# Kernel optimization log

Hardware: AMD Instinct MI355X
Metric: run time of the kernel (lower is better)

## Reference

```python
import jax, jax.numpy as jnp
import numpy as np

ALL_PERMS = jnp.array([[0, 1, 2], [0, 2, 1], [1, 0, 2], [1, 2, 0], [2, 0, 1], [2, 1, 0]], dtype=jnp.int32)
ENRICH_CLIP = 100.0
B, D, H = 16384, 512, 512
P_IN = D + 6 + 3   # seq_embed + pres_state(6) + round_onehot(3)
F_IN = D + 12 + 3  # seq_embed + full_state(12) + round_onehot(3)


def _gelu(x):
    return jax.nn.gelu(x, approximate=False)  # keras 'gelu' is erf-based


def _mlp3(x, w1, b1, w2, b2, w3, b3):
    h = _gelu(x @ w1 + b1)
    h = _gelu(h @ w2 + b2)
    return h @ w3 + b3


def setup_inputs() -> dict:
    key = jax.random.key(0)
    ks = jax.random.split(key, 12)
    s = 0.02
    return {
        'seq_embed': jax.random.normal(ks[0], (B, D), jnp.float32),
        'freq': jax.random.normal(ks[1], (B, 3), jnp.float32),
        'pres': (jax.random.uniform(ks[2], (B, 3)) < 0.5).astype(jnp.float32),
        'enrich': jax.random.normal(ks[3], (B, 3), jnp.float32),
        'pw1': jax.random.normal(ks[4], (P_IN, H), jnp.float32) * s, 'pb1': jnp.zeros((H,), jnp.float32),
        'pw2': jax.random.normal(ks[5], (H, H // 2), jnp.float32) * s, 'pb2': jnp.zeros((H // 2,), jnp.float32),
        'pw3': jax.random.normal(ks[6], (H // 2, 1), jnp.float32) * s, 'pb3': jnp.zeros((1,), jnp.float32),
        'fw1': jax.random.normal(ks[7], (F_IN, H), jnp.float32) * s, 'fb1': jnp.zeros((H,), jnp.float32),
        'fw2': jax.random.normal(ks[8], (H, H), jnp.float32) * s, 'fb2': jnp.zeros((H,), jnp.float32),
        'fw3': jax.random.normal(ks[9], (H, 2), jnp.float32) * s, 'fb3': jnp.zeros((2,), jnp.float32),
        'perm_idx': jax.random.randint(ks[10], (B,), 0, 6, dtype=jnp.int32),
        'round_mask': jax.random.randint(ks[11], (B, 3), 0, 2, dtype=jnp.int32),
    }


def _decode(seq_embed, freq, pres, enrich, mask_f, perms,
            pw1, pb1, pw2, pb2, pw3, pb3, fw1, fb1, fw2, fb2, fw3, fb3):
    Bn = seq_embed.shape[0]
    dt = seq_embed.dtype
    ones = jnp.ones((Bn,), dt)
    pres_state = jnp.zeros((Bn, 3, 2), dt)  # [R, (pres, decoded_flag)]
    full_state = jnp.zeros((Bn, 3, 4), dt)  # [R, (freq, pres, enrich, decoded_flag)]
    d_f = jnp.zeros((Bn, 3), dt)
    d_p = jnp.zeros((Bn, 3), dt)
    d_e = jnp.zeros((Bn, 3), dt)
    lf = lp = le = nm = jnp.float32(0.0)
    for step in range(3):
        ridx = perms[:, step]                               # [B]
        r_oh = jax.nn.one_hot(ridx, 3, dtype=dt)            # [B,3]
        take = lambda a: jnp.take_along_axis(a, ridx[:, None], axis=1)[:, 0]
        gt_f, gt_p, gt_e, m = take(freq), take(pres), take(enrich), take(mask_f)
        pres_inp = jnp.concatenate([seq_embed, pres_state.reshape(Bn, 6), r_oh], axis=1)
        pp_logit = _mlp3(pres_inp, pw1, pb1, pw2, pb2, pw3, pb3)[:, 0]
        fe_inp = jnp.concatenate([seq_embed, full_state.reshape(Bn, 12), r_oh], axis=1)
        fe_pred = _mlp3(fe_inp, fw1, fb1, fw2, fb2, fw3, fb3)
        pf, pe = fe_pred[:, 0], fe_pred[:, 1]
        lf = lf + jnp.sum(jnp.square(pf - gt_f) * m)
        bce = jnp.maximum(pp_logit, 0.0) - pp_logit * gt_p + jnp.log1p(jnp.exp(-jnp.abs(pp_logit)))
        lp = lp + jnp.sum(bce * m)
        le = le + jnp.sum(jnp.square(pe - gt_e) * m)
        nm = nm + jnp.sum(m)
        msk = m > 0.5
        act_f = jnp.where(msk, jnp.clip(pf, -10.0, 10.0), gt_f)
        act_p = jnp.where(msk, jax.nn.sigmoid(pp_logit), gt_p)
        act_e = jnp.where(msk, jnp.clip(pe, -ENRICH_CLIP, ENRICH_CLIP), gt_e)
        sel = r_oh[:, :, None]  # equal-mask scatter into the ridx-th slot
        pres_state = pres_state * (1.0 - sel) + jnp.stack([act_p, ones], axis=1)[:, None, :] * sel
        full_state = full_state * (1.0 - sel) + jnp.stack([act_f, act_p, act_e, ones], axis=1)[:, None, :] * sel
        d_f = d_f * (1.0 - r_oh) + act_f[:, None] * r_oh
        d_p = d_p * (1.0 - r_oh) + act_p[:, None] * r_oh
        d_e = d_e * (1.0 - r_oh) + act_e[:, None] * r_oh
    nm = nm + 1e-08
    return lf / nm, lp / nm, le / nm, d_f, d_p, d_e


def reference(seq_embed, freq, pres, enrich,
              pw1, pb1, pw2, pb2, pw3, pb3,
              fw1, fb1, fw2, fb2, fw3, fb3,
              perm_idx, round_mask):
    perms = ALL_PERMS[perm_idx]                      # [B,3] random round orders
    mask_f = round_mask.astype(seq_embed.dtype)      # [B,3] 0/1 mask
    lf, lp, le, d_f, d_p, d_e = _decode(seq_embed, freq, pres, enrich, mask_f, perms,
                                        pw1, pb1, pw2, pb2, pw3, pb3,
                                        fw1, fb1, fw2, fb2, fw3, fb3)
    # flat layout: [loss_freq, loss_pres, loss_enrich, dec_freq(B*3), dec_pres(B*3), dec_enrich(B*3)]
    return jnp.concatenate([jnp.stack([lf, lp, le]), d_f.ravel(), d_p.ravel(), d_e.ravel()])
```

## Files before the change

kernel.cpp:

```cpp
#include <hip/hip_runtime.h>
#include <hip/hip_bf16.h>
#include <math.h>

#define BATCH 16384

typedef unsigned short u16;
typedef short bf16x8 __attribute__((ext_vector_type(8)));
typedef float f32x4 __attribute__((ext_vector_type(4)));
typedef u16 u16x8 __attribute__((ext_vector_type(8)));
typedef u16 u16x4 __attribute__((ext_vector_type(4)));

__constant__ int PERMS_C[6][3] = {{0,1,2},{0,2,1},{1,0,2},{1,2,0},{2,0,1},{2,1,0}};

__device__ inline float bf2f(u16 u) {
    unsigned int x = ((unsigned int)u) << 16;
    float f; __builtin_memcpy(&f, &x, 4); return f;
}
__device__ inline u16 f2bf(float f) {
    __hip_bfloat16 h = __float2bfloat16(f);
    u16 u; __builtin_memcpy(&u, &h, 2); return u;
}
__device__ inline float gelu_exact(float x) {
    return 0.5f * x * (1.0f + erff(x * 0.70710678118654752f));
}

__device__ inline void gload_lds16(const u16* g, u16* l) {
    __builtin_amdgcn_global_load_lds(
        (const __attribute__((address_space(1))) unsigned int*)g,
        (__attribute__((address_space(3))) unsigned int*)l,
        16, 0, 0);
}

__global__ __launch_bounds__(256) void prep_kernel(
    const float* __restrict__ seq,
    const float* __restrict__ pw1, const float* __restrict__ pw2,
    const float* __restrict__ fw1, const float* __restrict__ fw2,
    const float* __restrict__ pb1, const float* __restrict__ pb2,
    const float* __restrict__ fb1, const float* __restrict__ fb2,
    u16* __restrict__ sb, u16* __restrict__ W1T, u16* __restrict__ W2T,
    float* __restrict__ bias1, float* __restrict__ bias2,
    float* __restrict__ states)
{
    const int N0 = BATCH * 512;
    const int N1 = 1024 * 512;
    const int N2 = 768 * 512;
    const int N3 = 1024;
    const int N4 = 768;
    const int N5 = BATCH * 18;
    int i = blockIdx.x * 256 + threadIdx.x;
    if (i < N0) { sb[i] = f2bf(seq[i]); return; }
    i -= N0;
    if (i < N1) {
        int n = i >> 9, k = i & 511;
        float v = (n < 512) ? pw1[(size_t)k * 512 + n] : fw1[(size_t)k * 512 + (n - 512)];
        W1T[i] = f2bf(v); return;
    }
    i -= N1;
    if (i < N2) {
        int n = i >> 9, k = i & 511;
        float v = (n < 256) ? pw2[(size_t)k * 256 + n] : fw2[(size_t)k * 512 + (n - 256)];
        W2T[i] = f2bf(v); return;
    }
    i -= N2;
    if (i < N3) { bias1[i] = (i < 512) ? pb1[i] : fb1[i - 512]; return; }
    i -= N3;
    if (i < N4) { bias2[i] = (i < 256) ? pb2[i] : fb2[i - 256]; return; }
    i -= N4;
    if (i < N5) { states[i] = 0.0f; return; }
}

__global__ __launch_bounds__(256) void gemm_bf16(
    const u16* __restrict__ A0, const u16* __restrict__ A1, int lda,
    const u16* __restrict__ Bt, const float* __restrict__ bias,
    u16* __restrict__ C, int M, int N, int K, int n_split, int apply_gelu)
{
    __shared__ __align__(16) u16 As[128 * 64];
    __shared__ __align__(16) u16 Bs[128 * 64];

    const int bm = blockIdx.x * 128;
    const int bn = blockIdx.y * 128;
    const u16* __restrict__ A = (bn < n_split) ? A0 : A1;

    const int tid = threadIdx.x;
    const int wv = tid >> 6;
    const int lane = tid & 63;
    const int wr = wv >> 1;
    const int wc = wv & 1;

    const int lrow = lane >> 3;
    const int lcol = (lane & 7) << 3;

    f32x4 acc[4][4];
#pragma unroll
    for (int i = 0; i < 4; ++i)
#pragma unroll
        for (int j = 0; j < 4; ++j) acc[i][j] = (f32x4){0.f, 0.f, 0.f, 0.f};

    for (int k0 = 0; k0 < K; k0 += 64) {
#pragma unroll
        for (int q = 0; q < 4; ++q) {
            const int c = wv * 4 + q;
            const int row = c * 8 + lrow;
            gload_lds16(&A[(size_t)(bm + row) * lda + k0 + lcol], &As[c * 512]);
            gload_lds16(&Bt[(size_t)(bn + row) * K + k0 + lcol], &Bs[c * 512]);
        }
        __syncthreads();

#pragma unroll
        for (int ks = 0; ks < 64; ks += 32) {
            int kk = ks + (lane >> 4) * 8;
            bf16x8 af[4], bfr[4];
#pragma unroll
            for (int i = 0; i < 4; ++i)
                af[i] = *reinterpret_cast<const bf16x8*>(&As[(wr * 64 + i * 16 + (lane & 15)) * 64 + kk]);
#pragma unroll
            for (int j = 0; j < 4; ++j)
                bfr[j] = *reinterpret_cast<const bf16x8*>(&Bs[(wc * 64 + j * 16 + (lane & 15)) * 64 + kk]);
#pragma unroll
            for (int i = 0; i < 4; ++i)
#pragma unroll
                for (int j = 0; j < 4; ++j)
                    acc[i][j] = __builtin_amdgcn_mfma_f32_16x16x32_bf16(af[i], bfr[j], acc[i][j], 0, 0, 0);
        }
        __syncthreads();
    }

    const int r4 = (lane >> 4) * 4;
    const int cn = lane & 15;
#pragma unroll
    for (int i = 0; i < 4; ++i) {
#pragma unroll
        for (int j = 0; j < 4; ++j) {
            int gcol = bn + wc * 64 + j * 16 + cn;
            float bsv = bias[gcol];
#pragma unroll
            for (int r = 0; r < 4; ++r) {
                int grow = bm + wr * 64 + i * 16 + r4 + r;
                float v = acc[i][j][r] + bsv;
                if (apply_gelu) v = gelu_exact(v);
                C[(size_t)grow * N + gcol] = f2bf(v);
            }
        }
    }
}

template<int NSTATE>
__device__ inline void step_h1_body(
    const u16* __restrict__ Z, const float* __restrict__ wsrc,
    const float* __restrict__ state, const int* __restrict__ perm_idx, int step,
    u16* __restrict__ H1, int colBase)
{
    constexpr int NR = NSTATE + 3;
    const int tid = threadIdx.x;
    const int c64 = tid & 63;
    const int ws = tid >> 6;
    const int col0 = c64 * 8;

    float w[NR][8];
#pragma unroll
    for (int t = 0; t < NR; ++t) {
        float4 a = *reinterpret_cast<const float4*>(&wsrc[(size_t)t * 512 + col0]);
        float4 b = *reinterpret_cast<const float4*>(&wsrc[(size_t)t * 512 + col0 + 4]);
        w[t][0] = a.x; w[t][1] = a.y; w[t][2] = a.z; w[t][3] = a.w;
        w[t][4] = b.x; w[t][5] = b.y; w[t][6] = b.z; w[t][7] = b.w;
    }

    int row = blockIdx.x * 16 + ws;
#pragma unroll 2
    for (int i = 0; i < 4; ++i, row += 4) {
        const int ridx = PERMS_C[perm_idx[row]][step];
        float s0[NSTATE];
        if constexpr (NSTATE == 6) {
            float2 a = *reinterpret_cast<const float2*>(&state[row * 6]);
            float2 b = *reinterpret_cast<const float2*>(&state[row * 6 + 2]);
            float2 c = *reinterpret_cast<const float2*>(&state[row * 6 + 4]);
            s0[0] = a.x; s0[1] = a.y; s0[2] = b.x; s0[3] = b.y; s0[4] = c.x; s0[5] = c.y;
        } else {
            float4 a = *reinterpret_cast<const float4*>(&state[row * 12]);
            float4 b = *reinterpret_cast<const float4*>(&state[row * 12 + 4]);
            float4 c = *reinterpret_cast<const float4*>(&state[row * 12 + 8]);
            s0[0] = a.x; s0[1] = a.y; s0[2]  = a.z; s0[3]  = a.w;
            s0[4] = b.x; s0[5] = b.y; s0[6]  = b.z; s0[7]  = b.w;
            s0[8] = c.x; s0[9] = c.y; s0[10] = c.z; s0[11] = c.w;
        }
        u16x8 z = *reinterpret_cast<const u16x8*>(&Z[(size_t)row * 1024 + colBase + col0]);
        u16x8 o;
#pragma unroll
        for (int e = 0; e < 8; ++e) {
            float d = (ridx == 0) ? w[NSTATE][e]
                    : ((ridx == 1) ? w[NSTATE + 1][e] : w[NSTATE + 2][e]);
#pragma unroll
            for (int t = 0; t < NSTATE; ++t) d += s0[t] * w[t][e];
            o[e] = f2bf(gelu_exact(bf2f(z[e]) + d));
        }
        *reinterpret_cast<u16x8*>(&H1[(size_t)row * 1024 + colBase + col0]) = o;
    }
}

__global__ __launch_bounds__(256) void step_h1_both(
    const u16* __restrict__ Z,
    const float* __restrict__ pw1s, const float* __restrict__ fw1s,
    const float* __restrict__ pres_state, const float* __restrict__ full_state,
    const int* __restrict__ perm_idx, int step, u16* __restrict__ H1)
{
    if (blockIdx.y == 0)
        step_h1_body<6>(Z, pw1s, pres_state, perm_idx, step, H1, 0);
    else
        step_h1_body<12>(Z, fw1s, full_state, perm_idx, step, H1, 512);
}

__global__ __launch_bounds__(256) void step_head(
    const u16* __restrict__ H2,
    const float* __restrict__ pw3, const float* __restrict__ pb3,
    const float* __restrict__ fw3, const float* __restrict__ fb3,
    const float* __restrict__ freq, const float* __restrict__ presv,
    const float* __restrict__ enrich,
    const int* __restrict__ round_mask, const int* __restrict__ perm_idx, int step,
    float* __restrict__ pres_state, float* __restrict__ full_state,
    float* __restrict__ part, float* __restrict__ out)
{
    const int wid = threadIdx.x >> 6;
    const int lane = threadIdx.x & 63;
    const int row0 = blockIdx.x * 16;

    __shared__ float lg[16][4];

    float4 wp = *reinterpret_cast<const float4*>(&pw3[lane * 4]);
    float4 wa = *reinterpret_cast<const float4*>(&fw3[lane * 16]);
    float4 wb = *reinterpret_cast<const float4*>(&fw3[lane * 16 + 4]);
    float4 wc = *reinterpret_cast<const float4*>(&fw3[lane * 16 + 8]);
    float4 wd = *reinterpret_cast<const float4*>(&fw3[lane * 16 + 12]);

#pragma unroll
    for (int i = 0; i < 4; ++i) {
        const int r = wid * 4 + i;
        const int b = row0 + r;
        const u16* h2 = &H2[(size_t)b * 768];

        u16x4 hp = *reinterpret_cast<const u16x4*>(&h2[lane * 4]);
        float sp = bf2f(hp[0]) * wp.x + bf2f(hp[1]) * wp.y
                 + bf2f(hp[2]) * wp.z + bf2f(hp[3]) * wp.w;

        u16x8 hf = *reinterpret_cast<const u16x8*>(&h2[256 + lane * 8]);
        float h0 = bf2f(hf[0]), h1 = bf2f(hf[1]), h2v = bf2f(hf[2]), h3 = bf2f(hf[3]);
        float h4 = bf2f(hf[4]), h5 = bf2f(hf[5]), h6v = bf2f(hf[6]), h7 = bf2f(hf[7]);
        float sf = h0 * wa.x + h1 * wa.z + h2v * wb.x + h3 * wb.z
                 + h4 * wc.x + h5 * wc.z + h6v * wd.x + h7 * wd.z;
        float se = h0 * wa.y + h1 * wa.w + h2v * wb.y + h3 * wb.w
                 + h4 * wc.y + h5 * wc.w + h6v * wd.y + h7 * wd.w;

        for (int off = 32; off > 0; off >>= 1) {
            sp += __shfl_down(sp, off);
            sf += __shfl_down(sf, off);
            se += __shfl_down(se, off);
        }
        if (lane == 0) { lg[r][0] = sp; lg[r][1] = sf; lg[r][2] = se; }
    }
    __syncthreads();

    float lf = 0.f, bce = 0.f, le = 0.f, mm = 0.f;
    if (wid == 0) {
        if (lane < 16) {
            const int b = row0 + lane;
            float logit = lg[lane][0] + pb3[0];
            float pf    = lg[lane][1] + fb3[0];
            float pe    = lg[lane][2] + fb3[1];
            int ridx = PERMS_C[perm_idx[b]][step];
            float gt_f = freq[b * 3 + ridx];
            float gt_p = presv[b * 3 + ridx];
            float gt_e = enrich[b * 3 + ridx];
            float m = (float)round_mask[b * 3 + ridx];
            lf  = (pf - gt_f) * (pf - gt_f) * m;
            bce = (fmaxf(logit, 0.f) - logit * gt_p + log1pf(expf(-fabsf(logit)))) * m;
            le  = (pe - gt_e) * (pe - gt_e) * m;
            mm  = m;
            bool msk = m > 0.5f;
            float act_f = msk ? fminf(fmaxf(pf, -10.f), 10.f) : gt_f;
            float act_p = msk ? 1.f / (1.f + expf(-logit)) : gt_p;
            float act_e = msk ? fminf(fmaxf(pe, -100.f), 100.f) : gt_e;
            pres_state[b * 6 + ridx * 2 + 0] = act_p;
            pres_state[b * 6 + ridx * 2 + 1] = 1.f;
            full_state[b * 12 + ridx * 4 + 0] = act_f;
            full_state[b * 12 + ridx * 4 + 1] = act_p;
            full_state[b * 12 + ridx * 4 + 2] = act_e;
            full_state[b * 12 + ridx * 4 + 3] = 1.f;
            out[3 + b * 3 + ridx] = act_f;
            out[3 + 3 * BATCH + b * 3 + ridx] = act_p;
            out[3 + 6 * BATCH + b * 3 + ridx] = act_e;
        }
        for (int off = 8; off > 0; off >>= 1) {
            lf  += __shfl_down(lf, off);
            bce += __shfl_down(bce, off);
            le  += __shfl_down(le, off);
            mm  += __shfl_down(mm, off);
        }
        if (lane == 0) {
            float4 v; v.x = lf; v.y = bce; v.z = le; v.w = mm;
            *reinterpret_cast<float4*>(&part[blockIdx.x * 4]) = v;
        }
    }
}

#define HEAD_BLOCKS (BATCH / 16)

__global__ __launch_bounds__(256) void finalize_kernel(
    const float* __restrict__ part, float* __restrict__ out)
{
    __shared__ float red[4][4];
    const int nslots = 3 * HEAD_BLOCKS;
    float a0 = 0.f, a1 = 0.f, a2 = 0.f, a3 = 0.f;
    for (int j = threadIdx.x; j < nslots; j += 256) {
        float4 v = *reinterpret_cast<const float4*>(&part[j * 4]);
        a0 += v.x; a1 += v.y; a2 += v.z; a3 += v.w;
    }
    for (int off = 32; off > 0; off >>= 1) {
        a0 += __shfl_down(a0, off);
        a1 += __shfl_down(a1, off);
        a2 += __shfl_down(a2, off);
        a3 += __shfl_down(a3, off);
    }
    const int wid = threadIdx.x >> 6, lane = threadIdx.x & 63;
    if (lane == 0) { red[wid][0] = a0; red[wid][1] = a1; red[wid][2] = a2; red[wid][3] = a3; }
    __syncthreads();
    if (threadIdx.x == 0) {
        float s0 = 0.f, s1 = 0.f, s2 = 0.f, s3 = 0.f;
#pragma unroll
        for (int w2 = 0; w2 < 4; ++w2) {
            s0 += red[w2][0]; s1 += red[w2][1]; s2 += red[w2][2]; s3 += red[w2][3];
        }
        float nm = s3 + 1e-8f;
        out[0] = s0 / nm;
        out[1] = s1 / nm;
        out[2] = s2 / nm;
    }
}

extern "C" void kernel_launch(void* const* d_in, const int* in_sizes, int n_in,
                              void* d_out, int out_size, void* d_ws, size_t ws_size,
                              hipStream_t stream)
{
    const float* seq       = (const float*)d_in[0];
    const float* freq      = (const float*)d_in[1];
    const float* presv     = (const float*)d_in[2];
    const float* enrich    = (const float*)d_in[3];
    const float* pw1       = (const float*)d_in[4];
    const float* pb1       = (const float*)d_in[5];
    const float* pw2       = (const float*)d_in[6];
    const float* pb2       = (const float*)d_in[7];
    const float* pw3       = (const float*)d_in[8];
    const float* pb3       = (const float*)d_in[9];
    const float* fw1       = (const float*)d_in[10];
    const float* fb1       = (const float*)d_in[11];
    const float* fw2       = (const float*)d_in[12];
    const float* fb2       = (const float*)d_in[13];
    const float* fw3       = (const float*)d_in[14];
    const float* fb3       = (const float*)d_in[15];
    const int*   perm_idx  = (const int*)d_in[16];
    const int*   round_mask= (const int*)d_in[17];
    float* out = (float*)d_out;

    char* w = (char*)d_ws;
    u16* sb  = (u16*)w;  w += (size_t)BATCH * 512 * 2;
    u16* Z   = (u16*)w;  w += (size_t)BATCH * 1024 * 2;
    u16* H1  = (u16*)w;  w += (size_t)BATCH * 1024 * 2;
    u16* H2  = (u16*)w;  w += (size_t)BATCH * 768 * 2;
    u16* W1T = (u16*)w;  w += (size_t)1024 * 512 * 2;
    u16* W2T = (u16*)w;  w += (size_t)768 * 512 * 2;
    float* bias1 = (float*)w; w += 1024 * 4;
    float* bias2 = (float*)w; w += 768 * 4;
    float* states = (float*)w; w += (size_t)BATCH * 18 * 4;
    float* part   = (float*)w;
    float* pres_state = states;
    float* full_state = states + (size_t)BATCH * 6;

    {
        const int total = BATCH * 512 + 1024 * 512 + 768 * 512 + 1024 + 768 + BATCH * 18;
        int grid = (total + 255) / 256;
        prep_kernel<<<grid, 256, 0, stream>>>(seq, pw1, pw2, fw1, fw2, pb1, pb2, fb1, fb2,
                                              sb, W1T, W2T, bias1, bias2, states);
    }

    gemm_bf16<<<dim3(BATCH / 128, 1024 / 128), 256, 0, stream>>>(
        sb, sb, 512, W1T, bias1, Z, BATCH, 1024, 512, 1 << 30, 0);

    for (int s = 0; s < 3; ++s) {
        step_h1_both<<<dim3(BATCH / 16, 2), 256, 0, stream>>>(
            Z, pw1 + (size_t)512 * 512, fw1 + (size_t)512 * 512,
            pres_state, full_state, perm_idx, s, H1);

        gemm_bf16<<<dim3(BATCH / 128, 768 / 128), 256, 0, stream>>>(
            H1, H1 + 512, 1024, W2T, bias2, H2, BATCH, 768, 512, 256, 1);

        step_head<<<HEAD_BLOCKS, 256, 0, stream>>>(
            H2, pw3, pb3, fw3, fb3, freq, presv, enrich,
            round_mask, perm_idx, s, pres_state, full_state,
            part + (size_t)s * HEAD_BLOCKS * 4, out);
    }

    finalize_kernel<<<1, 256, 0, stream>>>(part, out);
}
```

Before: 392.6 us.

## Double-buffer GEMM LDS tiles with swizzle and fuse step-0 H1 into first GEMM

The bf16 GEMM now uses two 32-wide K buffers in LDS. The next tile's global-to-LDS load is issued before the MFMA work on the current tile, with a manual vmcnt wait, and an XOR swizzle on the LDS layout is meant to reduce bank conflicts. The first GEMM's epilogue also produces step-0 H1 directly: the state is all zeros at step 0, so it adds the round one-hot weight row chosen by perm[.,0] and applies GELU. This removes one step_h1 launch and its re-read of Z. The cost is an extra output write and added epilogue registers in that GEMM, plus a smaller K tile per barrier.

```diff
diff --git a/kernel.cpp b/kernel.cpp
--- a/kernel.cpp
+++ b/kernel.cpp
@@ -72,10 +72,12 @@
 __global__ __launch_bounds__(256) void gemm_bf16(
     const u16* __restrict__ A0, const u16* __restrict__ A1, int lda,
     const u16* __restrict__ Bt, const float* __restrict__ bias,
-    u16* __restrict__ C, int M, int N, int K, int n_split, int apply_gelu)
-{
-    __shared__ __align__(16) u16 As[128 * 64];
-    __shared__ __align__(16) u16 Bs[128 * 64];
+    u16* __restrict__ C, int M, int N, int K, int n_split, int apply_gelu,
+    const float* __restrict__ ohp, const float* __restrict__ ohf,
+    const int* __restrict__ perm, u16* __restrict__ H1out)
+{
+    __shared__ __align__(16) u16 As[2][128 * 32];
+    __shared__ __align__(16) u16 Bs[2][128 * 32];
 
     const int bm = blockIdx.x * 128;
     const int bn = blockIdx.y * 128;
@@ -87,8 +89,8 @@
     const int wr = wv >> 1;
     const int wc = wv & 1;
 
-    const int lrow = lane >> 3;
-    const int lcol = (lane & 7) << 3;
+    const int srow = lane >> 2;
+    const int scol = ((lane & 3) ^ ((lane >> 3) & 3)) << 3;
 
     f32x4 acc[4][4];
 #pragma unroll
@@ -96,39 +98,81 @@
 #pragma unroll
         for (int j = 0; j < 4; ++j) acc[i][j] = (f32x4){0.f, 0.f, 0.f, 0.f};
 
-    for (int k0 = 0; k0 < K; k0 += 64) {
-#pragma unroll
-        for (int q = 0; q < 4; ++q) {
-            const int c = wv * 4 + q;
-            const int row = c * 8 + lrow;
-            gload_lds16(&A[(size_t)(bm + row) * lda + k0 + lcol], &As[c * 512]);
-            gload_lds16(&Bt[(size_t)(bn + row) * K + k0 + lcol], &Bs[c * 512]);
-        }
-        __syncthreads();
-
-#pragma unroll
-        for (int ks = 0; ks < 64; ks += 32) {
-            int kk = ks + (lane >> 4) * 8;
-            bf16x8 af[4], bfr[4];
-#pragma unroll
-            for (int i = 0; i < 4; ++i)
-                af[i] = *reinterpret_cast<const bf16x8*>(&As[(wr * 64 + i * 16 + (lane & 15)) * 64 + kk]);
+    const int NT = K >> 5;
+
+#define STAGE(buf, k0)                                                         \
+    {                                                                          \
+        _Pragma("unroll")                                                      \
+        for (int q = 0; q < 2; ++q) {                                          \
+            const int c = wv * 2 + q;                                          \
+            const int row = c * 16 + srow;                                     \
+            gload_lds16(&A[(size_t)(bm + row) * lda + (k0) + scol],            \
+                        &As[buf][c * 512]);                                    \
+            gload_lds16(&Bt[(size_t)(bn + row) * K + (k0) + scol],             \
+                        &Bs[buf][c * 512]);                                    \
+        }                                                                      \
+    }
+
+    STAGE(0, 0);
+
+    const int kkr = (((lane >> 4) ^ ((lane >> 1) & 3)) << 3);
+    const int fr = lane & 15;
+
+    for (int t = 0; t < NT; ++t) {
+        const int cur = t & 1;
+        if (t + 1 < NT) {
+            STAGE(cur ^ 1, (t + 1) << 5);
+            asm volatile("s_waitcnt vmcnt(4)" ::: "memory");
+        } else {
+            asm volatile("s_waitcnt vmcnt(0)" ::: "memory");
+        }
+        __builtin_amdgcn_sched_barrier(0);
+        __builtin_amdgcn_s_barrier();
+
+        bf16x8 af[4], bfr[4];
+#pragma unroll
+        for (int i = 0; i < 4; ++i)
+            af[i] = *reinterpret_cast<const bf16x8*>(&As[cur][(wr * 64 + i * 16 + fr) * 32 + kkr]);
+#pragma unroll
+        for (int j = 0; j < 4; ++j)
+            bfr[j] = *reinterpret_cast<const bf16x8*>(&Bs[cur][(wc * 64 + j * 16 + fr) * 32 + kkr]);
+#pragma unroll
+        for (int i = 0; i < 4; ++i)
 #pragma unroll
             for (int j = 0; j < 4; ++j)
-                bfr[j] = *reinterpret_cast<const bf16x8*>(&Bs[(wc * 64 + j * 16 + (lane & 15)) * 64 + kk]);
-#pragma unroll
-            for (int i = 0; i < 4; ++i)
-#pragma unroll
-                for (int j = 0; j < 4; ++j)
-                    acc[i][j] = __builtin_amdgcn_mfma_f32_16x16x32_bf16(af[i], bfr[j], acc[i][j], 0, 0, 0);
-        }
-        __syncthreads();
-    }
+                acc[i][j] = __builtin_amdgcn_mfma_f32_16x16x32_bf16(af[i], bfr[j], acc[i][j], 0, 0, 0);
+
+        __builtin_amdgcn_sched_barrier(0);
+        __builtin_amdgcn_s_barrier();
+    }
+#undef STAGE
 
     const int r4 = (lane >> 4) * 4;
     const int cn = lane & 15;
+
+    const float* ohb = nullptr;
+    float w0[4], w1[4], w2[4];
+    if (H1out) {
+        ohb = (bn < 512) ? (ohp + bn) : (ohf + (bn - 512));
+#pragma unroll
+        for (int j = 0; j < 4; ++j) {
+            int colw = wc * 64 + j * 16 + cn;
+            w0[j] = ohb[colw];
+            w1[j] = ohb[512 + colw];
+            w2[j] = ohb[1024 + colw];
+        }
+    }
+
 #pragma unroll
     for (int i = 0; i < 4; ++i) {
+        int rsel[4];
+        if (H1out) {
+#pragma unroll
+            for (int r = 0; r < 4; ++r) {
+                int grow = bm + wr * 64 + i * 16 + r4 + r;
+                rsel[r] = PERMS_C[perm[grow]][0];
+            }
+        }
 #pragma unroll
         for (int j = 0; j < 4; ++j) {
             int gcol = bn + wc * 64 + j * 16 + cn;
@@ -139,6 +183,10 @@
                 float v = acc[i][j][r] + bsv;
                 if (apply_gelu) v = gelu_exact(v);
                 C[(size_t)grow * N + gcol] = f2bf(v);
+                if (H1out) {
+                    float wv0 = (rsel[r] == 0) ? w0[j] : ((rsel[r] == 1) ? w1[j] : w2[j]);
+                    H1out[(size_t)grow * N + gcol] = f2bf(gelu_exact(v + wv0));
+                }
             }
         }
     }
@@ -381,15 +429,19 @@
     }
 
     gemm_bf16<<<dim3(BATCH / 128, 1024 / 128), 256, 0, stream>>>(
-        sb, sb, 512, W1T, bias1, Z, BATCH, 1024, 512, 1 << 30, 0);
+        sb, sb, 512, W1T, bias1, Z, BATCH, 1024, 512, 1 << 30, 0,
+        pw1 + (size_t)518 * 512, fw1 + (size_t)524 * 512, perm_idx, H1);
 
     for (int s = 0; s < 3; ++s) {
-        step_h1_both<<<dim3(BATCH / 16, 2), 256, 0, stream>>>(
-            Z, pw1 + (size_t)512 * 512, fw1 + (size_t)512 * 512,
-            pres_state, full_state, perm_idx, s, H1);
+        if (s > 0) {
+            step_h1_both<<<dim3(BATCH / 16, 2), 256, 0, stream>>>(
+                Z, pw1 + (size_t)512 * 512, fw1 + (size_t)512 * 512,
+                pres_state, full_state, perm_idx, s, H1);
+        }
 
         gemm_bf16<<<dim3(BATCH / 128, 768 / 128), 256, 0, stream>>>(
-            H1, H1 + 512, 1024, W2T, bias2, H2, BATCH, 768, 512, 256, 1);
+            H1, H1 + 512, 1024, W2T, bias2, H2, BATCH, 768, 512, 256, 1,
+            nullptr, nullptr, nullptr, nullptr);
 
         step_head<<<HEAD_BLOCKS, 256, 0, stream>>>(
             H2, pw3, pb3, fw3, fb3, freq, presv, enrich,
```

Result: faster. 364.0 us (-7.3%).

## Fuse three decode steps into one persistent kernel with H1 and state in LDS

Applied to the files above, without the earlier changes.

Replaces the per-step h1, second-layer GEMM and head kernels with a single decode3 kernel. Each 1024-thread block owns 64 rows and runs all three autoregressive steps. It keeps the H1 activations (XOR-swizzled) and the per-row decode state in LDS, and fuses the GELU and final projection into the MFMA epilogue. This removes the global H1/H2 round trips, the state buffers and nine kernel launches. In exchange it uses about 146KB of LDS, which allows only one block per CU, and it reads the W2T operand straight from global memory or cache without LDS staging.

```diff
diff --git a/kernel.cpp b/kernel.cpp
--- a/kernel.cpp
+++ b/kernel.cpp
@@ -8,7 +8,7 @@
 typedef short bf16x8 __attribute__((ext_vector_type(8)));
 typedef float f32x4 __attribute__((ext_vector_type(4)));
 typedef u16 u16x8 __attribute__((ext_vector_type(8)));
-typedef u16 u16x4 __attribute__((ext_vector_type(4)));
+typedef u16 u16x2 __attribute__((ext_vector_type(2)));
 
 __constant__ int PERMS_C[6][3] = {{0,1,2},{0,2,1},{1,0,2},{1,2,0},{2,0,1},{2,1,0}};
 
@@ -38,15 +38,13 @@
     const float* __restrict__ pb1, const float* __restrict__ pb2,
     const float* __restrict__ fb1, const float* __restrict__ fb2,
     u16* __restrict__ sb, u16* __restrict__ W1T, u16* __restrict__ W2T,
-    float* __restrict__ bias1, float* __restrict__ bias2,
-    float* __restrict__ states)
+    float* __restrict__ bias1, float* __restrict__ bias2)
 {
     const int N0 = BATCH * 512;
     const int N1 = 1024 * 512;
     const int N2 = 768 * 512;
     const int N3 = 1024;
     const int N4 = 768;
-    const int N5 = BATCH * 18;
     int i = blockIdx.x * 256 + threadIdx.x;
     if (i < N0) { sb[i] = f2bf(seq[i]); return; }
     i -= N0;
@@ -65,21 +63,18 @@
     if (i < N3) { bias1[i] = (i < 512) ? pb1[i] : fb1[i - 512]; return; }
     i -= N3;
     if (i < N4) { bias2[i] = (i < 256) ? pb2[i] : fb2[i - 256]; return; }
-    i -= N4;
-    if (i < N5) { states[i] = 0.0f; return; }
 }
 
 __global__ __launch_bounds__(256) void gemm_bf16(
-    const u16* __restrict__ A0, const u16* __restrict__ A1, int lda,
+    const u16* __restrict__ A, int lda,
     const u16* __restrict__ Bt, const float* __restrict__ bias,
-    u16* __restrict__ C, int M, int N, int K, int n_split, int apply_gelu)
+    u16* __restrict__ C, int M, int N, int K)
 {
     __shared__ __align__(16) u16 As[128 * 64];
     __shared__ __align__(16) u16 Bs[128 * 64];
 
     const int bm = blockIdx.x * 128;
     const int bn = blockIdx.y * 128;
-    const u16* __restrict__ A = (bn < n_split) ? A0 : A1;
 
     const int tid = threadIdx.x;
     const int wv = tid >> 6;
@@ -136,180 +131,261 @@
 #pragma unroll
             for (int r = 0; r < 4; ++r) {
                 int grow = bm + wr * 64 + i * 16 + r4 + r;
-                float v = acc[i][j][r] + bsv;
-                if (apply_gelu) v = gelu_exact(v);
-                C[(size_t)grow * N + gcol] = f2bf(v);
-            }
-        }
-    }
-}
-
-template<int NSTATE>
-__device__ inline void step_h1_body(
-    const u16* __restrict__ Z, const float* __restrict__ wsrc,
-    const float* __restrict__ state, const int* __restrict__ perm_idx, int step,
-    u16* __restrict__ H1, int colBase)
-{
-    constexpr int NR = NSTATE + 3;
-    const int tid = threadIdx.x;
-    const int c64 = tid & 63;
-    const int ws = tid >> 6;
-    const int col0 = c64 * 8;
-
-    float w[NR][8];
-#pragma unroll
-    for (int t = 0; t < NR; ++t) {
-        float4 a = *reinterpret_cast<const float4*>(&wsrc[(size_t)t * 512 + col0]);
-        float4 b = *reinterpret_cast<const float4*>(&wsrc[(size_t)t * 512 + col0 + 4]);
-        w[t][0] = a.x; w[t][1] = a.y; w[t][2] = a.z; w[t][3] = a.w;
-        w[t][4] = b.x; w[t][5] = b.y; w[t][6] = b.z; w[t][7] = b.w;
-    }
-
-    int row = blockIdx.x * 16 + ws;
-#pragma unroll 2
-    for (int i = 0; i < 4; ++i, row += 4) {
-        const int ridx = PERMS_C[perm_idx[row]][step];
-        float s0[NSTATE];
-        if constexpr (NSTATE == 6) {
-            float2 a = *reinterpret_cast<const float2*>(&state[row * 6]);
-            float2 b = *reinterpret_cast<const float2*>(&state[row * 6 + 2]);
-            float2 c = *reinterpret_cast<const float2*>(&state[row * 6 + 4]);
-            s0[0] = a.x; s0[1] = a.y; s0[2] = b.x; s0[3] = b.y; s0[4] = c.x; s0[5] = c.y;
+                C[(size_t)grow * N + gcol] = f2bf(acc[i][j][r] + bsv);
+            }
+        }
+    }
+}
+
+
+template<int NS>
+__device__ inline void h1_phase(
+    const float* __restrict__ wsrc, int cw0, int rh, int row0,
+    const u16* __restrict__ Z, int gcol0, char* h1base,
+    const float (*state)[20], const int* rid)
+{
+    float w[NS + 3][2];
+#pragma unroll
+    for (int r = 0; r < NS + 3; ++r) {
+        float2 v = *reinterpret_cast<const float2*>(&wsrc[(size_t)r * 512 + cw0]);
+        w[r][0] = v.x; w[r][1] = v.y;
+    }
+#pragma unroll 4
+    for (int r = 0; r < 32; ++r) {
+        const int row = rh * 32 + r;
+        const int ridx = rid[row];
+        float s[NS];
+        if constexpr (NS == 6) {
+            float4 a = *reinterpret_cast<const float4*>(&state[row][0]);
+            float2 b = *reinterpret_cast<const float2*>(&state[row][4]);
+            s[0] = a.x; s[1] = a.y; s[2] = a.z; s[3] = a.w; s[4] = b.x; s[5] = b.y;
         } else {
-            float4 a = *reinterpret_cast<const float4*>(&state[row * 12]);
-            float4 b = *reinterpret_cast<const float4*>(&state[row * 12 + 4]);
-            float4 c = *reinterpret_cast<const float4*>(&state[row * 12 + 8]);
-            s0[0] = a.x; s0[1] = a.y; s0[2]  = a.z; s0[3]  = a.w;
-            s0[4] = b.x; s0[5] = b.y; s0[6]  = b.z; s0[7]  = b.w;
-            s0[8] = c.x; s0[9] = c.y; s0[10] = c.z; s0[11] = c.w;
-        }
-        u16x8 z = *reinterpret_cast<const u16x8*>(&Z[(size_t)row * 1024 + colBase + col0]);
-        u16x8 o;
-#pragma unroll
-        for (int e = 0; e < 8; ++e) {
-            float d = (ridx == 0) ? w[NSTATE][e]
-                    : ((ridx == 1) ? w[NSTATE + 1][e] : w[NSTATE + 2][e]);
-#pragma unroll
-            for (int t = 0; t < NSTATE; ++t) d += s0[t] * w[t][e];
-            o[e] = f2bf(gelu_exact(bf2f(z[e]) + d));
-        }
-        *reinterpret_cast<u16x8*>(&H1[(size_t)row * 1024 + colBase + col0]) = o;
-    }
-}
-
-__global__ __launch_bounds__(256) void step_h1_both(
+            float4 a = *reinterpret_cast<const float4*>(&state[row][8]);
+            float4 b = *reinterpret_cast<const float4*>(&state[row][12]);
+            float4 c = *reinterpret_cast<const float4*>(&state[row][16]);
+            s[0] = a.x; s[1] = a.y; s[2]  = a.z; s[3]  = a.w;
+            s[4] = b.x; s[5] = b.y; s[6]  = b.z; s[7]  = b.w;
+            s[8] = c.x; s[9] = c.y; s[10] = c.z; s[11] = c.w;
+        }
+        u16x2 z = *reinterpret_cast<const u16x2*>(&Z[(size_t)(row0 + row) * 1024 + gcol0]);
+        float d0 = (ridx == 0) ? w[NS][0] : ((ridx == 1) ? w[NS + 1][0] : w[NS + 2][0]);
+        float d1 = (ridx == 0) ? w[NS][1] : ((ridx == 1) ? w[NS + 1][1] : w[NS + 2][1]);
+#pragma unroll
+        for (int j = 0; j < NS; ++j) { d0 += s[j] * w[j][0]; d1 += s[j] * w[j][1]; }
+        float h0 = gelu_exact(bf2f(z[0]) + d0);
+        float h1 = gelu_exact(bf2f(z[1]) + d1);
+        unsigned int packed = (unsigned int)f2bf(h0) | ((unsigned int)f2bf(h1) << 16);
+        int byte = (row * 2048 + gcol0 * 2) ^ ((row & 7) << 4);
+        *reinterpret_cast<unsigned int*>(h1base + byte) = packed;
+    }
+}
+
+__global__ __launch_bounds__(1024, 4) void decode3(
     const u16* __restrict__ Z,
     const float* __restrict__ pw1s, const float* __restrict__ fw1s,
-    const float* __restrict__ pres_state, const float* __restrict__ full_state,
-    const int* __restrict__ perm_idx, int step, u16* __restrict__ H1)
-{
-    if (blockIdx.y == 0)
-        step_h1_body<6>(Z, pw1s, pres_state, perm_idx, step, H1, 0);
-    else
-        step_h1_body<12>(Z, fw1s, full_state, perm_idx, step, H1, 512);
-}
-
-__global__ __launch_bounds__(256) void step_head(
-    const u16* __restrict__ H2,
+    const u16* __restrict__ W2T, const float* __restrict__ bias2,
     const float* __restrict__ pw3, const float* __restrict__ pb3,
     const float* __restrict__ fw3, const float* __restrict__ fb3,
     const float* __restrict__ freq, const float* __restrict__ presv,
-    const float* __restrict__ enrich,
-    const int* __restrict__ round_mask, const int* __restrict__ perm_idx, int step,
-    float* __restrict__ pres_state, float* __restrict__ full_state,
+    const float* __restrict__ enrich, const int* __restrict__ round_mask,
+    const int* __restrict__ perm_idx,
     float* __restrict__ part, float* __restrict__ out)
 {
-    const int wid = threadIdx.x >> 6;
-    const int lane = threadIdx.x & 63;
-    const int row0 = blockIdx.x * 16;
-
-    __shared__ float lg[16][4];
-
-    float4 wp = *reinterpret_cast<const float4*>(&pw3[lane * 4]);
-    float4 wa = *reinterpret_cast<const float4*>(&fw3[lane * 16]);
-    float4 wb = *reinterpret_cast<const float4*>(&fw3[lane * 16 + 4]);
-    float4 wc = *reinterpret_cast<const float4*>(&fw3[lane * 16 + 8]);
-    float4 wd = *reinterpret_cast<const float4*>(&fw3[lane * 16 + 12]);
-
-#pragma unroll
-    for (int i = 0; i < 4; ++i) {
-        const int r = wid * 4 + i;
-        const int b = row0 + r;
-        const u16* h2 = &H2[(size_t)b * 768];
-
-        u16x4 hp = *reinterpret_cast<const u16x4*>(&h2[lane * 4]);
-        float sp = bf2f(hp[0]) * wp.x + bf2f(hp[1]) * wp.y
-                 + bf2f(hp[2]) * wp.z + bf2f(hp[3]) * wp.w;
-
-        u16x8 hf = *reinterpret_cast<const u16x8*>(&h2[256 + lane * 8]);
-        float h0 = bf2f(hf[0]), h1 = bf2f(hf[1]), h2v = bf2f(hf[2]), h3 = bf2f(hf[3]);
-        float h4 = bf2f(hf[4]), h5 = bf2f(hf[5]), h6v = bf2f(hf[6]), h7 = bf2f(hf[7]);
-        float sf = h0 * wa.x + h1 * wa.z + h2v * wb.x + h3 * wb.z
-                 + h4 * wc.x + h5 * wc.z + h6v * wd.x + h7 * wd.z;
-        float se = h0 * wa.y + h1 * wa.w + h2v * wb.y + h3 * wb.w
-                 + h4 * wc.y + h5 * wc.w + h6v * wd.y + h7 * wd.w;
-
-        for (int off = 32; off > 0; off >>= 1) {
-            sp += __shfl_down(sp, off);
-            sf += __shfl_down(sf, off);
-            se += __shfl_down(se, off);
-        }
-        if (lane == 0) { lg[r][0] = sp; lg[r][1] = sf; lg[r][2] = se; }
+    __shared__ __align__(16) u16 H1s[64 * 1024];
+    __shared__ float redh[16][64][3];
+    __shared__ __align__(16) float state_s[64][20];
+    __shared__ int pidx_s[64];
+    __shared__ int rid_s[64];
+
+    const int tid = threadIdx.x;
+    const int wv  = tid >> 6;
+    const int l   = tid & 63;
+    const int row0 = blockIdx.x * 64;
+
+    {
+        float* ss = &state_s[0][0];
+        for (int i = tid; i < 64 * 20; i += 1024) ss[i] = 0.f;
+        if (tid < 64) {
+            int pp = perm_idx[row0 + tid];
+            pidx_s[tid] = pp;
+            rid_s[tid] = PERMS_C[pp][0];
+        }
     }
     __syncthreads();
 
-    float lf = 0.f, bce = 0.f, le = 0.f, mm = 0.f;
-    if (wid == 0) {
-        if (lane < 16) {
-            const int b = row0 + lane;
-            float logit = lg[lane][0] + pb3[0];
-            float pf    = lg[lane][1] + fb3[0];
-            float pe    = lg[lane][2] + fb3[1];
-            int ridx = PERMS_C[perm_idx[b]][step];
+    const int ci   = tid & 511;
+    const int rh   = tid >> 9;
+    const int half = ci >> 8;
+    const int cw0  = (ci & 255) * 2;
+    const int gcol0 = ci * 2;
+    char* h1base = reinterpret_cast<char*>(H1s);
+
+    const int colbase = wv * 48;
+    const bool needP = (colbase < 256);
+    const bool needF = (colbase + 32) >= 256;
+
+    float lf_acc = 0.f, bce_acc = 0.f, le_acc = 0.f, mm_acc = 0.f;
+
+#pragma unroll 1
+    for (int step = 0; step < 3; ++step) {
+        if (half == 0)
+            h1_phase<6>(pw1s, cw0, rh, row0, Z, gcol0, h1base, state_s, rid_s);
+        else
+            h1_phase<12>(fw1s, cw0, rh, row0, Z, gcol0, h1base, state_s, rid_s);
+        __syncthreads();
+
+        f32x4 acc[4][3];
+#pragma unroll
+        for (int rf = 0; rf < 4; ++rf)
+#pragma unroll
+            for (int cf = 0; cf < 3; ++cf) acc[rf][cf] = (f32x4){0.f, 0.f, 0.f, 0.f};
+
+        const int ar = l & 15;
+        const int ks = (l >> 4) * 8;
+#pragma unroll 2
+        for (int kf = 0; kf < 16; ++kf) {
+            bf16x8 bfr[3];
+#pragma unroll
+            for (int cf = 0; cf < 3; ++cf) {
+                int col = colbase + cf * 16 + ar;
+                bfr[cf] = *reinterpret_cast<const bf16x8*>(&W2T[(size_t)col * 512 + kf * 32 + ks]);
+            }
+            bf16x8 afP[4], afF[4];
+            if (needP) {
+#pragma unroll
+                for (int rf = 0; rf < 4; ++rf) {
+                    int row = rf * 16 + ar;
+                    int byte = (row * 2048 + (kf * 32 + ks) * 2) ^ ((row & 7) << 4);
+                    afP[rf] = *reinterpret_cast<const bf16x8*>(h1base + byte);
+                }
+            }
+            if (needF) {
+#pragma unroll
+                for (int rf = 0; rf < 4; ++rf) {
+                    int row = rf * 16 + ar;
+                    int byte = (row * 2048 + 1024 + (kf * 32 + ks) * 2) ^ ((row & 7) << 4);
+                    afF[rf] = *reinterpret_cast<const bf16x8*>(h1base + byte);
+                }
+            }
+#pragma unroll
+            for (int cf = 0; cf < 3; ++cf) {
+                const bool hf = (colbase + cf * 16) >= 256;
+#pragma unroll
+                for (int rf = 0; rf < 4; ++rf)
+                    acc[rf][cf] = __builtin_amdgcn_mfma_f32_16x16x32_bf16(
+                        hf ? afF[rf] : afP[rf], bfr[cf], acc[rf][cf], 0, 0, 0);
+            }
+        }
+
+#pragma unroll
+        for (int rf = 0; rf < 4; ++rf) {
+            float hsp[4] = {0.f, 0.f, 0.f, 0.f};
+            float hsf[4] = {0.f, 0.f, 0.f, 0.f};
+            float hse[4] = {0.f, 0.f, 0.f, 0.f};
+#pragma unroll
+            for (int cf = 0; cf < 3; ++cf) {
+                const int colc = colbase + cf * 16;
+                const int col = colc + ar;
+                const float b2 = bias2[col];
+                if (colc < 256) {
+                    const float w3 = pw3[col];
+#pragma unroll
+                    for (int g = 0; g < 4; ++g) {
+                        float h = gelu_exact(acc[rf][cf][g] + b2);
+                        hsp[g] += h * w3;
+                    }
+                } else {
+                    const float wf = fw3[(col - 256) * 2];
+                    const float we = fw3[(col - 256) * 2 + 1];
+#pragma unroll
+                    for (int g = 0; g < 4; ++g) {
+                        float h = gelu_exact(acc[rf][cf][g] + b2);
+                        hsf[g] += h * wf;
+                        hse[g] += h * we;
+                    }
+                }
+            }
+#pragma unroll
+            for (int g = 0; g < 4; ++g) {
+                float a = hsp[g], b = hsf[g], c = hse[g];
+#pragma unroll
+                for (int m = 1; m < 16; m <<= 1) {
+                    a += __shfl_xor(a, m);
+                    b += __shfl_xor(b, m);
+                    c += __shfl_xor(c, m);
+                }
+                if ((l & 15) == 0) {
+                    int row = rf * 16 + (l >> 4) * 4 + g;
+                    redh[wv][row][0] = a;
+                    redh[wv][row][1] = b;
+                    redh[wv][row][2] = c;
+                }
+            }
+        }
+        __syncthreads();
+
+        if (wv == 0) {
+            const int row = l;
+            const int b = row0 + row;
+            float sp = 0.f, sf = 0.f, se = 0.f;
+#pragma unroll
+            for (int w2 = 0; w2 < 16; ++w2) {
+                sp += redh[w2][row][0];
+                sf += redh[w2][row][1];
+                se += redh[w2][row][2];
+            }
+            float logit = sp + pb3[0];
+            float pf    = sf + fb3[0];
+            float pe    = se + fb3[1];
+            int ridx = rid_s[row];
             float gt_f = freq[b * 3 + ridx];
             float gt_p = presv[b * 3 + ridx];
             float gt_e = enrich[b * 3 + ridx];
             float m = (float)round_mask[b * 3 + ridx];
-            lf  = (pf - gt_f) * (pf - gt_f) * m;
-            bce = (fmaxf(logit, 0.f) - logit * gt_p + log1pf(expf(-fabsf(logit)))) * m;
-            le  = (pe - gt_e) * (pe - gt_e) * m;
-            mm  = m;
+            lf_acc  += (pf - gt_f) * (pf - gt_f) * m;
+            bce_acc += (fmaxf(logit, 0.f) - logit * gt_p + log1pf(expf(-fabsf(logit)))) * m;
+            le_acc  += (pe - gt_e) * (pe - gt_e) * m;
+            mm_acc  += m;
             bool msk = m > 0.5f;
             float act_f = msk ? fminf(fmaxf(pf, -10.f), 10.f) : gt_f;
             float act_p = msk ? 1.f / (1.f + expf(-logit)) : gt_p;
             float act_e = msk ? fminf(fmaxf(pe, -100.f), 100.f) : gt_e;
-            pres_state[b * 6 + ridx * 2 + 0] = act_p;
-            pres_state[b * 6 + ridx * 2 + 1] = 1.f;
-            full_state[b * 12 + ridx * 4 + 0] = act_f;
-            full_state[b * 12 + ridx * 4 + 1] = act_p;
-            full_state[b * 12 + ridx * 4 + 2] = act_e;
-            full_state[b * 12 + ridx * 4 + 3] = 1.f;
+            state_s[row][ridx * 2 + 0] = act_p;
+            state_s[row][ridx * 2 + 1] = 1.f;
+            state_s[row][8 + ridx * 4 + 0] = act_f;
+            state_s[row][8 + ridx * 4 + 1] = act_p;
+            state_s[row][8 + ridx * 4 + 2] = act_e;
+            state_s[row][8 + ridx * 4 + 3] = 1.f;
             out[3 + b * 3 + ridx] = act_f;
             out[3 + 3 * BATCH + b * 3 + ridx] = act_p;
             out[3 + 6 * BATCH + b * 3 + ridx] = act_e;
-        }
-        for (int off = 8; off > 0; off >>= 1) {
-            lf  += __shfl_down(lf, off);
-            bce += __shfl_down(bce, off);
-            le  += __shfl_down(le, off);
-            mm  += __shfl_down(mm, off);
-        }
-        if (lane == 0) {
-            float4 v; v.x = lf; v.y = bce; v.z = le; v.w = mm;
+            if (step < 2) rid_s[row] = PERMS_C[pidx_s[row]][step + 1];
+        }
+        __syncthreads();
+    }
+
+    if (wv == 0) {
+        for (int off = 32; off > 0; off >>= 1) {
+            lf_acc  += __shfl_down(lf_acc, off);
+            bce_acc += __shfl_down(bce_acc, off);
+            le_acc  += __shfl_down(le_acc, off);
+            mm_acc  += __shfl_down(mm_acc, off);
+        }
+        if (l == 0) {
+            float4 v; v.x = lf_acc; v.y = bce_acc; v.z = le_acc; v.w = mm_acc;
             *reinterpret_cast<float4*>(&part[blockIdx.x * 4]) = v;
         }
     }
 }
 
-#define HEAD_BLOCKS (BATCH / 16)
+#define NPART (BATCH / 64)
 
 __global__ __launch_bounds__(256) void finalize_kernel(
     const float* __restrict__ part, float* __restrict__ out)
 {
     __shared__ float red[4][4];
-    const int nslots = 3 * HEAD_BLOCKS;
     float a0 = 0.f, a1 = 0.f, a2 = 0.f, a3 = 0.f;
-    for (int j = threadIdx.x; j < nslots; j += 256) {
+    for (int j = threadIdx.x; j < NPART; j += 256) {
         float4 v = *reinterpret_cast<const float4*>(&part[j * 4]);
         a0 += v.x; a1 += v.y; a2 += v.z; a3 += v.w;
     }
@@ -362,40 +438,26 @@
     char* w = (char*)d_ws;
     u16* sb  = (u16*)w;  w += (size_t)BATCH * 512 * 2;
     u16* Z   = (u16*)w;  w += (size_t)BATCH * 1024 * 2;
-    u16* H1  = (u16*)w;  w += (size_t)BATCH * 1024 * 2;
-    u16* H2  = (u16*)w;  w += (size_t)BATCH * 768 * 2;
     u16* W1T = (u16*)w;  w += (size_t)1024 * 512 * 2;
     u16* W2T = (u16*)w;  w += (size_t)768 * 512 * 2;
     float* bias1 = (float*)w; w += 1024 * 4;
     float* bias2 = (float*)w; w += 768 * 4;
-    float* states = (float*)w; w += (size_t)BATCH * 18 * 4;
-    float* part   = (float*)w;
-    float* pres_state = states;
-    float* full_state = states + (size_t)BATCH * 6;
+    float* part  = (float*)w;
 
     {
-        const int total = BATCH * 512 + 1024 * 512 + 768 * 512 + 1024 + 768 + BATCH * 18;
+        const int total = BATCH * 512 + 1024 * 512 + 768 * 512 + 1024 + 768;
         int grid = (total + 255) / 256;
         prep_kernel<<<grid, 256, 0, stream>>>(seq, pw1, pw2, fw1, fw2, pb1, pb2, fb1, fb2,
-                                              sb, W1T, W2T, bias1, bias2, states);
+                                              sb, W1T, W2T, bias1, bias2);
     }
 
     gemm_bf16<<<dim3(BATCH / 128, 1024 / 128), 256, 0, stream>>>(
-        sb, sb, 512, W1T, bias1, Z, BATCH, 1024, 512, 1 << 30, 0);
-
-    for (int s = 0; s < 3; ++s) {
-        step_h1_both<<<dim3(BATCH / 16, 2), 256, 0, stream>>>(
-            Z, pw1 + (size_t)512 * 512, fw1 + (size_t)512 * 512,
-            pres_state, full_state, perm_idx, s, H1);
-
-        gemm_bf16<<<dim3(BATCH / 128, 768 / 128), 256, 0, stream>>>(
-            H1, H1 + 512, 1024, W2T, bias2, H2, BATCH, 768, 512, 256, 1);
-
-        step_head<<<HEAD_BLOCKS, 256, 0, stream>>>(
-            H2, pw3, pb3, fw3, fb3, freq, presv, enrich,
-            round_mask, perm_idx, s, pres_state, full_state,
-            part + (size_t)s * HEAD_BLOCKS * 4, out);
-    }
+        sb, 512, W1T, bias1, Z, BATCH, 1024, 512);
+
+    decode3<<<NPART, 1024, 0, stream>>>(
+        Z, pw1 + (size_t)512 * 512, fw1 + (size_t)512 * 512,
+        W2T, bias2, pw3, pb3, fw3, fb3,
+        freq, presv, enrich, round_mask, perm_idx, part, out);
 
     finalize_kernel<<<1, 256, 0, stream>>>(part, out);
 }
```

Measured after the change: 349.8 us. -10.9%, faster.
